# Optimization experiments

Hardware: AMD Instinct MI355X
Metric: run time of the kernel (lower is better)

The kernel has to match this reference:

```python
import jax, jax.numpy as jnp
import numpy as np

NEG_SLOPE = 0.2  # PyG GATConv default leaky_relu slope
EPS = 1e-16     # PyG softmax denominator epsilon


def gat_conv(x, src, dst, edge_attr, W, att_src, att_dst, W_edge, att_edge, bias):
    """Single-head PyG GATConv with edge_dim. x:[N,Fin] -> [N,Fout].
    src/dst already include self-loops; edge_attr matches their length."""
    N = x.shape[0]
    h = x @ W                      # [N, Fout] transformed node features
    a_s = h @ att_src              # [N] per-node source logit contribution
    a_d = h @ att_dst              # [N]
    a_e = (edge_attr @ W_edge) @ att_edge   # [E] edge contribution
    logits = jax.nn.leaky_relu(a_s[src] + a_d[dst] + a_e, NEG_SLOPE)  # [E]
    # segment softmax over destination nodes
    m = jax.ops.segment_max(logits, dst, num_segments=N)    # [N]
    m = jnp.where(jnp.isfinite(m), m, 0.0)
    e = jnp.exp(logits - m[dst])                             # [E]
    denom = jax.ops.segment_sum(e, dst, num_segments=N)      # [N]
    alpha = e / (denom[dst] + EPS)                            # [E]
    # scatter-aggregate weighted messages
    out = jax.ops.segment_sum(alpha[:, None] * h[src], dst, num_segments=N)
    return out + bias


def setup_inputs() -> dict:
    key = jax.random.key(0)
    ks = jax.random.split(key, 16)
    N, E, F_in, H, C, ED = 100000, 1600000, 128, 64, 2, 1
    inp = {
        "x": jax.random.normal(ks[0], (N, F_in), dtype=jnp.float32),
        "edge_index": jax.random.randint(ks[1], (2, E), 0, N, dtype=jnp.int32),
        "edge_attr": jax.random.normal(ks[2], (E, ED), dtype=jnp.float32),
        # layer 1 params (Glorot-ish scale)
        "W1": jax.random.normal(ks[3], (F_in, H), dtype=jnp.float32) * (1.0 / np.sqrt(F_in)),
        "att_src1": jax.random.normal(ks[4], (H,), dtype=jnp.float32) * (1.0 / np.sqrt(H)),
        "att_dst1": jax.random.normal(ks[5], (H,), dtype=jnp.float32) * (1.0 / np.sqrt(H)),
        "W_edge1": jax.random.normal(ks[6], (ED, H), dtype=jnp.float32),
        "att_edge1": jax.random.normal(ks[7], (H,), dtype=jnp.float32) * (1.0 / np.sqrt(H)),
        "bias1": jnp.zeros((H,), dtype=jnp.float32),
        # layer 2 params
        "W2": jax.random.normal(ks[8], (H, C), dtype=jnp.float32) * (1.0 / np.sqrt(H)),
        "att_src2": jax.random.normal(ks[9], (C,), dtype=jnp.float32),
        "att_dst2": jax.random.normal(ks[10], (C,), dtype=jnp.float32),
        "W_edge2": jax.random.normal(ks[11], (ED, C), dtype=jnp.float32),
        "att_edge2": jax.random.normal(ks[12], (C,), dtype=jnp.float32),
        "bias2": jnp.zeros((C,), dtype=jnp.float32),
    }
    return inp


def reference(x, edge_index, edge_attr,
              W1, att_src1, att_dst1, W_edge1, att_edge1, bias1,
              W2, att_src2, att_dst2, W_edge2, att_edge2, bias2):
    N = x.shape[0]
    # PyG GATConv add_self_loops=True, fill_value='mean' for edge_attr
    loop = jnp.arange(N, dtype=edge_index.dtype)
    src = jnp.concatenate([edge_index[0], loop])
    dst = jnp.concatenate([edge_index[1], loop])
    ea_mean = jnp.mean(edge_attr, axis=0, keepdims=True)              # [1, ED]
    ea = jnp.concatenate([edge_attr, jnp.broadcast_to(ea_mean, (N, edge_attr.shape[1]))])

    h = gat_conv(x, src, dst, ea, W1, att_src1, att_dst1, W_edge1, att_edge1, bias1)
    h = jax.nn.relu(h)  # dropout is identity in eval mode
    out = gat_conv(h, src, dst, ea, W2, att_src2, att_dst2, W_edge2, att_edge2, bias2)
    return jax.nn.log_softmax(out, axis=1)
```

## Files before the change

### kernel.cpp

```cpp
#include <hip/hip_runtime.h>
#include <math.h>

#define NEG_SLOPE 0.2f
#define EPSF 1e-16f

constexpr int FIN = 128;
constexpr int H   = 64;
constexpr int C   = 2;
constexpr int BSHIFT = 8;
constexpr int NBUCK_MAX = 1024;
constexpr int CHUNK = 4096;
constexpr int CAP   = 6144;

typedef short v8s __attribute__((ext_vector_type(8)));
typedef float v4f __attribute__((ext_vector_type(4)));
typedef unsigned short u16;

__device__ inline void split_bf16(float v, u16& hi, u16& lo) {
    unsigned u = __float_as_uint(v);
    unsigned r = (u + 0x7FFFu + ((u >> 16) & 1u)) >> 16;
    hi = (u16)r;
    float hf = __uint_as_float(r << 16);
    float l = v - hf;
    unsigned ul = __float_as_uint(l);
    lo = (u16)((ul + 0x7FFFu + ((ul >> 16) & 1u)) >> 16);
}

__device__ inline u16 to_bf16(float v) {
    unsigned u = __float_as_uint(v);
    return (u16)((u + 0x7FFFu + ((u >> 16) & 1u)) >> 16);
}
__device__ inline float blo(int v) { return __uint_as_float((unsigned)v << 16); }
__device__ inline float bhi(int v) { return __uint_as_float((unsigned)v & 0xFFFF0000u); }

__device__ inline int scan1024_excl(int v, int* wtot, int t) {
    int lane = t & 63, w = t >> 6;
    int incl = v;
    #pragma unroll
    for (int o = 1; o < 64; o <<= 1) {
        int u = __shfl_up(incl, o, 64);
        if (lane >= o) incl += u;
    }
    if (lane == 63) wtot[w] = incl;
    __syncthreads();
    int woff = 0;
    for (int i = 0; i < w; i++) woff += wtot[i];
    return woff + incl - v;
}

__global__ __launch_bounds__(1024) void fused_pre_gemm_kernel(
        const float* __restrict__ ea, const int* __restrict__ dst, int E,
        float* __restrict__ csum, int* __restrict__ cnt, int* __restrict__ bcount,
        const float* __restrict__ x, const float* __restrict__ W1,
        const float* __restrict__ att_src, const float* __restrict__ att_dst,
        u16* __restrict__ h1b, float* __restrict__ a_s, float* __restrict__ a_d,
        int N, int NBUCK, int NCHUNK) {
    int t = threadIdx.x;
    if ((int)blockIdx.x < NCHUNK) {
        __shared__ int lh[NBUCK_MAX];
        __shared__ float wsum[16];
        int c = blockIdx.x;
        lh[t] = 0;
        __syncthreads();
        int base = c * CHUNK;
        int cntE = min(CHUNK, E - base);
        float acc = 0.f;
        for (int i = t; i < cntE; i += 1024) {
            int e = base + i;
            acc += ea[e];
            atomicAdd(&lh[dst[e] >> BSHIFT], 1);
        }
        for (int off = 32; off; off >>= 1) acc += __shfl_down(acc, off, 64);
        int lane = t & 63, wv = t >> 6;
        if (lane == 0) wsum[wv] = acc;
        __syncthreads();
        if (t == 0) {
            float s = 0.f;
            #pragma unroll
            for (int i = 0; i < 16; i++) s += wsum[i];
            csum[c] = s;
        }
        if (t < NBUCK) {
            int v = lh[t];
            cnt[(size_t)c * NBUCK + t] = v;
            if (v) atomicAdd(&bcount[t], v);
        }
        return;
    }
    __shared__ u16 WhL[FIN * H];
    __shared__ u16 WlL[FIN * H];
    int bid = blockIdx.x - NCHUNK;
    int w = t >> 6, lane = t & 63;
    int m = lane & 15, q = lane >> 4;
    int base = bid * 256 + w * 16;
    int nodeA = base + m;
    bool inA = nodeA < N;
    const float* xrow = x + (size_t)nodeA * FIN;

    float w1v[8];
    #pragma unroll
    for (int j = 0; j < 8; j++) w1v[j] = W1[t + j * 1024];
    float4 xv4[8];
    #pragma unroll
    for (int kt = 0; kt < 4; kt++) {
        if (inA) {
            const float4* p = (const float4*)(xrow + kt * 32 + q * 8);
            xv4[kt * 2]     = p[0];
            xv4[kt * 2 + 1] = p[1];
        } else {
            xv4[kt * 2]     = make_float4(0.f, 0.f, 0.f, 0.f);
            xv4[kt * 2 + 1] = make_float4(0.f, 0.f, 0.f, 0.f);
        }
    }
    #pragma unroll
    for (int j = 0; j < 8; j++) {
        int gid = t + j * 1024;
        int k = gid >> 6, f = gid & 63;
        u16 hb, lb;
        split_bf16(w1v[j], hb, lb);
        int idx = ((k >> 3) << 9) + (f << 3) + (k & 7);
        WhL[idx] = hb;
        WlL[idx] = lb;
    }
    v8s ah[4], al[4];
    #pragma unroll
    for (int kt = 0; kt < 4; kt++) {
        float xv[8];
        xv[0] = xv4[kt * 2].x;     xv[1] = xv4[kt * 2].y;
        xv[2] = xv4[kt * 2].z;     xv[3] = xv4[kt * 2].w;
        xv[4] = xv4[kt * 2 + 1].x; xv[5] = xv4[kt * 2 + 1].y;
        xv[6] = xv4[kt * 2 + 1].z; xv[7] = xv4[kt * 2 + 1].w;
        #pragma unroll
        for (int j = 0; j < 8; j++) {
            u16 hb, lb;
            split_bf16(xv[j], hb, lb);
            ah[kt][j] = (short)hb;
            al[kt][j] = (short)lb;
        }
    }
    __syncthreads();

    float ps[4] = {0.f, 0.f, 0.f, 0.f};
    float pd[4] = {0.f, 0.f, 0.f, 0.f};
    #pragma unroll
    for (int ft = 0; ft < 4; ft++) {
        v4f acc = {0.f, 0.f, 0.f, 0.f};
        #pragma unroll
        for (int kt = 0; kt < 4; kt++) {
            int fi = ((kt * 4 + q) << 9) + ((ft * 16 + m) << 3);
            v8s bh = *(const v8s*)(WhL + fi);
            v8s bl = *(const v8s*)(WlL + fi);
            acc = __builtin_amdgcn_mfma_f32_16x16x32_bf16(ah[kt], bh, acc, 0, 0, 0);
            acc = __builtin_amdgcn_mfma_f32_16x16x32_bf16(al[kt], bh, acc, 0, 0, 0);
            acc = __builtin_amdgcn_mfma_f32_16x16x32_bf16(ah[kt], bl, acc, 0, 0, 0);
        }
        int f = ft * 16 + m;
        float asf = att_src[f], adf = att_dst[f];
        #pragma unroll
        for (int r = 0; r < 4; r++) {
            int node = base + q * 4 + r;
            if (node < N) h1b[(size_t)node * H + f] = to_bf16(acc[r]);
            ps[r] += acc[r] * asf;
            pd[r] += acc[r] * adf;
        }
    }
    #pragma unroll
    for (int msk = 1; msk < 16; msk <<= 1) {
        #pragma unroll
        for (int r = 0; r < 4; r++) {
            ps[r] += __shfl_xor(ps[r], msk, 64);
            pd[r] += __shfl_xor(pd[r], msk, 64);
        }
    }
    if (m == 0) {
        #pragma unroll
        for (int r = 0; r < 4; r++) {
            int node = base + q * 4 + r;
            if (node < N) { a_s[node] = ps[r]; a_d[node] = pd[r]; }
        }
    }
}

__global__ __launch_bounds__(1024) void stage_kernel(
        const int* __restrict__ src, const int* __restrict__ dst, const float* __restrict__ ea,
        int E, const int* __restrict__ cnt, const int* __restrict__ bcount,
        int* __restrict__ gcur,
        int2* __restrict__ staging, int* __restrict__ bbase_out, int NBUCK, int NCHUNK,
        const float* __restrict__ csum,
        const float* __restrict__ W_edge1, const float* __restrict__ att_edge1,
        const float* __restrict__ W_edge2, const float* __restrict__ att_edge2,
        float* __restrict__ scal, int* __restrict__ rowN) {
    __shared__ int   bb[NBUCK_MAX];
    __shared__ int   cur[NBUCK_MAX];
    __shared__ int   gofs[NBUCK_MAX];
    __shared__ int2  sbuf[CHUNK];
    __shared__ short sbkt[CHUNK];
    __shared__ int   wt16[16];
    __shared__ float ws16[16];
    int t = threadIdx.x;
    int c = blockIdx.x;
    int base = c * CHUNK;
    int cntE = min(CHUNK, E - base);
    int bv = (t < NBUCK) ? bcount[t] : 0;
    int bx = scan1024_excl(bv, wt16, t);
    if (t < NBUCK) bb[t] = bx;
    if (c == 0) {
        if (t < NBUCK) bbase_out[t] = bx;
        if (t == 0) { bbase_out[NBUCK] = E; *rowN = E; }
        float acc = 0.f;
        for (int i = t; i < NCHUNK; i += 1024) acc += csum[i];
        for (int off = 32; off; off >>= 1) acc += __shfl_down(acc, off, 64);
        if ((t & 63) == 0) ws16[t >> 6] = acc;
    }
    __syncthreads();
    if (c == 0 && t == 0) {
        float tot = 0.f;
        #pragma unroll
        for (int i = 0; i < 16; i++) tot += ws16[i];
        float c1 = 0.f;
        for (int i = 0; i < H; i++) c1 += W_edge1[i] * att_edge1[i];
        float c2 = 0.f;
        for (int i = 0; i < C; i++) c2 += W_edge2[i] * att_edge2[i];
        scal[0] = tot / (float)E; scal[1] = c1; scal[2] = c2;
    }
    int h = (t < NBUCK) ? cnt[(size_t)c * NBUCK + t] : 0;
    int p = scan1024_excl(h, wt16, t);
    if (t < NBUCK) {
        if (h) gofs[t] = bb[t] + atomicAdd(&gcur[t], h) - p;
        cur[t] = p;
    }
    __syncthreads();
    for (int i = t; i < cntE; i += 1024) {
        int e = base + i;
        int d = dst[e];
        int b = d >> BSHIFT;
        int slot = atomicAdd(&cur[b], 1);
        sbuf[slot] = make_int2(src[e] | ((d & ((1 << BSHIFT) - 1)) << 20), __float_as_int(ea[e]));
        sbkt[slot] = (short)b;
    }
    __syncthreads();
    for (int j = t; j < cntE; j += 1024)
        staging[gofs[sbkt[j]] + j] = sbuf[j];
}

__global__ __launch_bounds__(1024) void bfin_kernel(
        const int2* __restrict__ staging, const int* __restrict__ bbase,
        const float* __restrict__ scal,
        const float* __restrict__ a_s1, const float* __restrict__ a_d1,
        int* __restrict__ row, int2* __restrict__ sedge, float* __restrict__ sea2, int N) {
    __shared__ int   nh[256];
    __shared__ int   wt16[16];
    __shared__ int2  ebuf[CAP];
    __shared__ float abuf[CAP];
    int b = blockIdx.x, t = threadIdx.x;
    int beg = bbase[b], end = bbase[b + 1];
    int cnt = end - beg;
    int node0 = b << BSHIFT;
    float c1 = scal[1];
    if (t < 256) nh[t] = 0;
    __syncthreads();
    for (int i = beg + t; i < end; i += 1024)
        atomicAdd(&nh[(unsigned)staging[i].x >> 20], 1);
    __syncthreads();
    int v = (t < 256) ? nh[t] : 0;
    int lane = t & 63, w = t >> 6;
    int incl = v;
    #pragma unroll
    for (int o = 1; o < 64; o <<= 1) {
        int u = __shfl_up(incl, o, 64);
        if (lane >= o) incl += u;
    }
    if (w < 4 && lane == 63) wt16[w] = incl;
    __syncthreads();
    int woff = 0;
    int wl = w < 4 ? w : 4;
    for (int i = 0; i < wl; i++) woff += wt16[i];
    int excl = woff + incl - v;
    int node = node0 + t;
    if (t < 256 && node < N) row[node] = beg + excl;
    bool fast = (cnt <= CAP);
    if (t < 256) nh[t] = fast ? excl : beg + excl;
    __syncthreads();
    for (int i = beg + t; i < end; i += 1024) {
        int2 r = staging[i];
        int dlow = (unsigned)r.x >> 20;
        int sn = r.x & 0xFFFFF;
        float eav = __int_as_float(r.y);
        float lg = a_s1[sn] + a_d1[node0 + dlow] + eav * c1;
        lg = lg > 0.f ? lg : NEG_SLOPE * lg;
        float ex = __expf(lg);
        int pos = atomicAdd(&nh[dlow], 1);
        if (fast) {
            ebuf[pos] = make_int2(sn, __float_as_int(ex));
            abuf[pos] = eav;
        } else {
            sedge[pos] = make_int2(sn, __float_as_int(ex));
            sea2[pos] = eav;
        }
    }
    __syncthreads();
    if (fast) {
        for (int j = t; j < cnt; j += 1024) {
            sedge[beg + j] = ebuf[j];
            sea2[beg + j]  = abuf[j];
        }
    }
}

__device__ inline void accum8(float acc[8], float& den, float xw, int4 hv) {
    den += xw;
    acc[0] += xw * blo(hv.x); acc[1] += xw * bhi(hv.x);
    acc[2] += xw * blo(hv.y); acc[3] += xw * bhi(hv.y);
    acc[4] += xw * blo(hv.z); acc[5] += xw * bhi(hv.z);
    acc[6] += xw * blo(hv.w); acc[7] += xw * bhi(hv.w);
}

__global__ __launch_bounds__(256) void agg1_kernel(
        const int* __restrict__ row, const int2* __restrict__ sedge,
        const float* __restrict__ scal,
        const float* __restrict__ a_s, const float* __restrict__ a_d,
        const u16* __restrict__ h1b,
        const float* __restrict__ bias1, const float* __restrict__ W2,
        const float* __restrict__ att_src2, const float* __restrict__ att_dst2,
        float* __restrict__ h2, float* __restrict__ a_s2, float* __restrict__ a_d2,
        int N) {
    int wv = threadIdx.x >> 6;
    int lane = threadIdx.x & 63;
    int g  = lane >> 3;
    int fl = lane & 7;
    int n = blockIdx.x * 32 + wv * 8 + g;
    if (n >= N) return;
    int beg = row[n], end = row[n + 1];
    float den = 0.f;
    float acc[8] = {0.f, 0.f, 0.f, 0.f, 0.f, 0.f, 0.f, 0.f};
    const u16* hrow = h1b + fl * 8;
    int i = beg;
    for (; i + 4 <= end; i += 4) {
        int2 e0 = sedge[i], e1 = sedge[i + 1], e2 = sedge[i + 2], e3 = sedge[i + 3];
        int4 h0 = *(const int4*)(hrow + (size_t)e0.x * H);
        int4 h1v = *(const int4*)(hrow + (size_t)e1.x * H);
        int4 h2v = *(const int4*)(hrow + (size_t)e2.x * H);
        int4 h3v = *(const int4*)(hrow + (size_t)e3.x * H);
        accum8(acc, den, __int_as_float(e0.y), h0);
        accum8(acc, den, __int_as_float(e1.y), h1v);
        accum8(acc, den, __int_as_float(e2.y), h2v);
        accum8(acc, den, __int_as_float(e3.y), h3v);
    }
    if (i + 2 <= end) {
        int2 e0 = sedge[i], e1 = sedge[i + 1];
        int4 h0 = *(const int4*)(hrow + (size_t)e0.x * H);
        int4 h1v = *(const int4*)(hrow + (size_t)e1.x * H);
        accum8(acc, den, __int_as_float(e0.y), h0);
        accum8(acc, den, __int_as_float(e1.y), h1v);
        i += 2;
    }
    if (i < end) {
        int2 e0 = sedge[i];
        int4 h0 = *(const int4*)(hrow + (size_t)e0.x * H);
        accum8(acc, den, __int_as_float(e0.y), h0);
    }
    {
        float lg = a_s[n] + a_d[n] + scal[0] * scal[1];
        lg = lg > 0.f ? lg : NEG_SLOPE * lg;
        float ex = __expf(lg);
        int4 hs = *(const int4*)(hrow + (size_t)n * H);
        accum8(acc, den, ex, hs);
    }
    float inv = 1.f / (den + EPSF);
    float p0 = 0.f, p1 = 0.f;
    #pragma unroll
    for (int k = 0; k < 8; k++) {
        int f = fl * 8 + k;
        float hr = acc[k] * inv + bias1[f];
        hr = fmaxf(hr, 0.f);
        p0 += hr * W2[f * C + 0];
        p1 += hr * W2[f * C + 1];
    }
    #pragma unroll
    for (int msk = 1; msk < 8; msk <<= 1) {
        p0 += __shfl_xor(p0, msk, 64);
        p1 += __shfl_xor(p1, msk, 64);
    }
    if (fl == 0) {
        h2[(size_t)n * C + 0] = p0;
        h2[(size_t)n * C + 1] = p1;
        a_s2[n] = p0 * att_src2[0] + p1 * att_src2[1];
        a_d2[n] = p0 * att_dst2[0] + p1 * att_dst2[1];
    }
}

__global__ __launch_bounds__(256) void agg2_kernel(
        const int* __restrict__ row, const int2* __restrict__ sedge, const float* __restrict__ sea2,
        const float* __restrict__ scal,
        const float* __restrict__ a_s2, const float* __restrict__ a_d2,
        const float* __restrict__ h2, const float* __restrict__ bias2,
        float* __restrict__ out, int N) {
    int wv = threadIdx.x >> 6;
    int lane = threadIdx.x & 63;
    int g  = lane >> 3;
    int fl = lane & 7;
    int n = blockIdx.x * 32 + wv * 8 + g;
    if (n >= N) return;
    float c2 = scal[2];
    float ad = a_d2[n];
    int beg = row[n], end = row[n + 1];
    float den = 0.f, m0 = 0.f, m1 = 0.f;
    for (int i = beg + fl; i < end; i += 8) {
        int s = sedge[i].x;
        float lg = a_s2[s] + ad + sea2[i] * c2;
        lg = lg > 0.f ? lg : NEG_SLOPE * lg;
        float ex = __expf(lg);
        den += ex;
        m0 += ex * h2[(size_t)s * C + 0];
        m1 += ex * h2[(size_t)s * C + 1];
    }
    if (fl == 0) {
        float lg = a_s2[n] + ad + scal[0] * c2;
        lg = lg > 0.f ? lg : NEG_SLOPE * lg;
        float ex = __expf(lg);
        den += ex;
        m0 += ex * h2[(size_t)n * C + 0];
        m1 += ex * h2[(size_t)n * C + 1];
    }
    #pragma unroll
    for (int msk = 1; msk < 8; msk <<= 1) {
        den += __shfl_xor(den, msk, 64);
        m0  += __shfl_xor(m0, msk, 64);
        m1  += __shfl_xor(m1, msk, 64);
    }
    if (fl == 0) {
        float dn = den + EPSF;
        float o0 = m0 / dn + bias2[0];
        float o1 = m1 / dn + bias2[1];
        float mx = fmaxf(o0, o1);
        float lse = mx + logf(expf(o0 - mx) + expf(o1 - mx));
        out[(size_t)n * C + 0] = o0 - lse;
        out[(size_t)n * C + 1] = o1 - lse;
    }
}

extern "C" void kernel_launch(void* const* d_in, const int* in_sizes, int n_in,
                              void* d_out, int out_size, void* d_ws, size_t ws_size,
                              hipStream_t stream) {
    const float* x        = (const float*)d_in[0];
    const int*   ei       = (const int*)d_in[1];
    const float* ea       = (const float*)d_in[2];
    const float* W1       = (const float*)d_in[3];
    const float* att_src1 = (const float*)d_in[4];
    const float* att_dst1 = (const float*)d_in[5];
    const float* W_edge1  = (const float*)d_in[6];
    const float* att_edge1= (const float*)d_in[7];
    const float* bias1    = (const float*)d_in[8];
    const float* W2       = (const float*)d_in[9];
    const float* att_src2 = (const float*)d_in[10];
    const float* att_dst2 = (const float*)d_in[11];
    const float* W_edge2  = (const float*)d_in[12];
    const float* att_edge2= (const float*)d_in[13];
    const float* bias2    = (const float*)d_in[14];

    const int N  = in_sizes[0] / FIN;
    const int E  = in_sizes[1] / 2;
    const int* srcp = ei;
    const int* dstp = ei + E;
    const int NBUCK  = (N + (1 << BSHIFT) - 1) >> BSHIFT;
    const int NCHUNK = (E + CHUNK - 1) / CHUNK;
    const int NGEMM  = (N + 255) / 256;

    char* wsb = (char*)d_ws;
    size_t off = 0;
    auto alloc = [&](size_t bytes) { void* p = wsb + off; off += (bytes + 255) & ~size_t(255); return p; };
    int*   bcount = (int*)alloc((size_t)NBUCK_MAX * 4);
    int*   gcur   = (int*)alloc((size_t)NBUCK_MAX * 4);
    size_t zbytes = off;
    float* csum   = (float*)alloc((size_t)2048 * 4);
    int*   bbase  = (int*)alloc((size_t)(NBUCK_MAX + 1) * 4);
    int*   cnt    = (int*)alloc((size_t)NCHUNK * NBUCK * 4);
    int*   row    = (int*)alloc((size_t)(N + 1) * 4);
    int2*  sedge  = (int2*)alloc((size_t)(E + 8) * 8);
    float* sea2   = (float*)alloc((size_t)E * 4);
    int2*  staging= (int2*)alloc((size_t)E * 8);
    u16*   h1b    = (u16*)alloc((size_t)N * H * 2);
    float* a_s1   = (float*)alloc((size_t)N * 4);
    float* a_d1   = (float*)alloc((size_t)N * 4);
    float* h2     = (float*)alloc((size_t)N * C * 4);
    float* a_s2   = (float*)alloc((size_t)N * 4);
    float* a_d2   = (float*)alloc((size_t)N * 4);
    float* scal   = (float*)alloc(3 * 4);

    hipMemsetAsync(d_ws, 0, zbytes, stream);

    fused_pre_gemm_kernel<<<NCHUNK + NGEMM, 1024, 0, stream>>>(
        ea, dstp, E, csum, cnt, bcount,
        x, W1, att_src1, att_dst1, h1b, a_s1, a_d1, N, NBUCK, NCHUNK);
    stage_kernel<<<NCHUNK, 1024, 0, stream>>>(
        srcp, dstp, ea, E, cnt, bcount, gcur, staging, bbase, NBUCK, NCHUNK,
        csum, W_edge1, att_edge1, W_edge2, att_edge2, scal, row + N);
    bfin_kernel<<<NBUCK, 1024, 0, stream>>>(staging, bbase, scal, a_s1, a_d1, row, sedge, sea2, N);
    agg1_kernel<<<(N + 31) / 32, 256, 0, stream>>>(row, sedge, scal, a_s1, a_d1, h1b,
                                                   bias1, W2, att_src2, att_dst2,
                                                   h2, a_s2, a_d2, N);
    agg2_kernel<<<(N + 31) / 32, 256, 0, stream>>>(row, sedge, sea2, scal, a_s2, a_d2, h2, bias2,
                                                   (float*)d_out, N);
}
```

Before: 226.8 us.

## Split layer-1 GEMM into separate 256-thread kernel with pre-split bf16 weights

The layer-1 MFMA GEMM no longer shares a launch with the histogram blocks. The pre kernel now writes W1 once to global memory as hi/lo bf16 halves in MFMA layout, and a new 256-thread GEMM kernel copies those halves into LDS with vector loads. This removes the per-block W1 split and lets smaller blocks raise occupancy. In exchange it adds a kernel launch, puts the GEMM after the staging kernel instead of overlapping it with the histogram, and each block still loads 32KB of weights for only 64 nodes.

```diff
diff --git a/kernel.cpp b/kernel.cpp
--- a/kernel.cpp
+++ b/kernel.cpp
@@ -48,136 +48,49 @@
     return woff + incl - v;
 }
 
-__global__ __launch_bounds__(1024) void fused_pre_gemm_kernel(
-        const float* __restrict__ ea, const int* __restrict__ dst, int E,
-        float* __restrict__ csum, int* __restrict__ cnt, int* __restrict__ bcount,
-        const float* __restrict__ x, const float* __restrict__ W1,
-        const float* __restrict__ att_src, const float* __restrict__ att_dst,
-        u16* __restrict__ h1b, float* __restrict__ a_s, float* __restrict__ a_d,
-        int N, int NBUCK, int NCHUNK) {
-    int t = threadIdx.x;
-    if ((int)blockIdx.x < NCHUNK) {
-        __shared__ int lh[NBUCK_MAX];
-        __shared__ float wsum[16];
-        int c = blockIdx.x;
-        lh[t] = 0;
-        __syncthreads();
-        int base = c * CHUNK;
-        int cntE = min(CHUNK, E - base);
-        float acc = 0.f;
-        for (int i = t; i < cntE; i += 1024) {
-            int e = base + i;
-            acc += ea[e];
-            atomicAdd(&lh[dst[e] >> BSHIFT], 1);
-        }
-        for (int off = 32; off; off >>= 1) acc += __shfl_down(acc, off, 64);
-        int lane = t & 63, wv = t >> 6;
-        if (lane == 0) wsum[wv] = acc;
-        __syncthreads();
-        if (t == 0) {
-            float s = 0.f;
-            #pragma unroll
-            for (int i = 0; i < 16; i++) s += wsum[i];
-            csum[c] = s;
-        }
-        if (t < NBUCK) {
-            int v = lh[t];
-            cnt[(size_t)c * NBUCK + t] = v;
-            if (v) atomicAdd(&bcount[t], v);
-        }
-        return;
-    }
-    __shared__ u16 WhL[FIN * H];
-    __shared__ u16 WlL[FIN * H];
-    int bid = blockIdx.x - NCHUNK;
-    int w = t >> 6, lane = t & 63;
-    int m = lane & 15, q = lane >> 4;
-    int base = bid * 256 + w * 16;
-    int nodeA = base + m;
-    bool inA = nodeA < N;
-    const float* xrow = x + (size_t)nodeA * FIN;
-
-    float w1v[8];
-    #pragma unroll
-    for (int j = 0; j < 8; j++) w1v[j] = W1[t + j * 1024];
-    float4 xv4[8];
-    #pragma unroll
-    for (int kt = 0; kt < 4; kt++) {
-        if (inA) {
-            const float4* p = (const float4*)(xrow + kt * 32 + q * 8);
-            xv4[kt * 2]     = p[0];
-            xv4[kt * 2 + 1] = p[1];
-        } else {
-            xv4[kt * 2]     = make_float4(0.f, 0.f, 0.f, 0.f);
-            xv4[kt * 2 + 1] = make_float4(0.f, 0.f, 0.f, 0.f);
-        }
-    }
-    #pragma unroll
-    for (int j = 0; j < 8; j++) {
-        int gid = t + j * 1024;
+__global__ __launch_bounds__(1024) void pre_kernel(const float* __restrict__ ea,
+                                                   const int* __restrict__ dst, int E,
+                                                   float* __restrict__ csum, int* __restrict__ cnt,
+                                                   int* __restrict__ bcount,
+                                                   const float* __restrict__ W1,
+                                                   u16* __restrict__ Wt_hi, u16* __restrict__ Wt_lo,
+                                                   int NBUCK) {
+    int c = blockIdx.x, t = threadIdx.x;
+    int gid = c * 1024 + t;
+    if (gid < FIN * H) {
         int k = gid >> 6, f = gid & 63;
-        u16 hb, lb;
-        split_bf16(w1v[j], hb, lb);
+        u16 h, l;
+        split_bf16(W1[gid], h, l);
         int idx = ((k >> 3) << 9) + (f << 3) + (k & 7);
-        WhL[idx] = hb;
-        WlL[idx] = lb;
-    }
-    v8s ah[4], al[4];
-    #pragma unroll
-    for (int kt = 0; kt < 4; kt++) {
-        float xv[8];
-        xv[0] = xv4[kt * 2].x;     xv[1] = xv4[kt * 2].y;
-        xv[2] = xv4[kt * 2].z;     xv[3] = xv4[kt * 2].w;
-        xv[4] = xv4[kt * 2 + 1].x; xv[5] = xv4[kt * 2 + 1].y;
-        xv[6] = xv4[kt * 2 + 1].z; xv[7] = xv4[kt * 2 + 1].w;
-        #pragma unroll
-        for (int j = 0; j < 8; j++) {
-            u16 hb, lb;
-            split_bf16(xv[j], hb, lb);
-            ah[kt][j] = (short)hb;
-            al[kt][j] = (short)lb;
-        }
-    }
-    __syncthreads();
-
-    float ps[4] = {0.f, 0.f, 0.f, 0.f};
-    float pd[4] = {0.f, 0.f, 0.f, 0.f};
-    #pragma unroll
-    for (int ft = 0; ft < 4; ft++) {
-        v4f acc = {0.f, 0.f, 0.f, 0.f};
-        #pragma unroll
-        for (int kt = 0; kt < 4; kt++) {
-            int fi = ((kt * 4 + q) << 9) + ((ft * 16 + m) << 3);
-            v8s bh = *(const v8s*)(WhL + fi);
-            v8s bl = *(const v8s*)(WlL + fi);
-            acc = __builtin_amdgcn_mfma_f32_16x16x32_bf16(ah[kt], bh, acc, 0, 0, 0);
-            acc = __builtin_amdgcn_mfma_f32_16x16x32_bf16(al[kt], bh, acc, 0, 0, 0);
-            acc = __builtin_amdgcn_mfma_f32_16x16x32_bf16(ah[kt], bl, acc, 0, 0, 0);
-        }
-        int f = ft * 16 + m;
-        float asf = att_src[f], adf = att_dst[f];
-        #pragma unroll
-        for (int r = 0; r < 4; r++) {
-            int node = base + q * 4 + r;
-            if (node < N) h1b[(size_t)node * H + f] = to_bf16(acc[r]);
-            ps[r] += acc[r] * asf;
-            pd[r] += acc[r] * adf;
-        }
-    }
-    #pragma unroll
-    for (int msk = 1; msk < 16; msk <<= 1) {
-        #pragma unroll
-        for (int r = 0; r < 4; r++) {
-            ps[r] += __shfl_xor(ps[r], msk, 64);
-            pd[r] += __shfl_xor(pd[r], msk, 64);
-        }
-    }
-    if (m == 0) {
-        #pragma unroll
-        for (int r = 0; r < 4; r++) {
-            int node = base + q * 4 + r;
-            if (node < N) { a_s[node] = ps[r]; a_d[node] = pd[r]; }
-        }
+        Wt_hi[idx] = h;
+        Wt_lo[idx] = l;
+    }
+    __shared__ int lh[NBUCK_MAX];
+    __shared__ float wsum[16];
+    lh[t] = 0;
+    __syncthreads();
+    int base = c * CHUNK;
+    int cntE = min(CHUNK, E - base);
+    float acc = 0.f;
+    for (int i = t; i < cntE; i += 1024) {
+        int e = base + i;
+        acc += ea[e];
+        atomicAdd(&lh[dst[e] >> BSHIFT], 1);
+    }
+    for (int off = 32; off; off >>= 1) acc += __shfl_down(acc, off, 64);
+    int lane = t & 63, wv = t >> 6;
+    if (lane == 0) wsum[wv] = acc;
+    __syncthreads();
+    if (t == 0) {
+        float s = 0.f;
+        #pragma unroll
+        for (int i = 0; i < 16; i++) s += wsum[i];
+        csum[c] = s;
+    }
+    if (t < NBUCK) {
+        int v = lh[t];
+        cnt[(size_t)c * NBUCK + t] = v;
+        if (v) atomicAdd(&bcount[t], v);
     }
 }
 
@@ -243,6 +156,112 @@
         staging[gofs[sbkt[j]] + j] = sbuf[j];
 }
 
+__global__ __launch_bounds__(256) void gemm1_mfma_kernel(
+        const float* __restrict__ x,
+        const u16* __restrict__ Wt_hi, const u16* __restrict__ Wt_lo,
+        const float* __restrict__ att_src, const float* __restrict__ att_dst,
+        u16* __restrict__ h1b, float* __restrict__ a_s, float* __restrict__ a_d, int N) {
+    __shared__ u16 WhL[FIN * H];
+    __shared__ u16 WlL[FIN * H];
+    int t = threadIdx.x;
+    int w = t >> 6, lane = t & 63;
+    int m = lane & 15, q = lane >> 4;
+    int base = blockIdx.x * 64 + w * 16;
+    int nodeA = base + m;
+    bool inA = nodeA < N;
+    const float* xrow = x + (size_t)nodeA * FIN;
+
+    float4 fh[4], fl4[4];
+    {
+        const float4* gh = (const float4*)Wt_hi;
+        const float4* gl = (const float4*)Wt_lo;
+        #pragma unroll
+        for (int i = 0; i < 4; i++) {
+            fh[i]  = gh[t + i * 256];
+            fl4[i] = gl[t + i * 256];
+        }
+    }
+    float4 xv4[8];
+    #pragma unroll
+    for (int kt = 0; kt < 4; kt++) {
+        if (inA) {
+            const float4* p = (const float4*)(xrow + kt * 32 + q * 8);
+            xv4[kt * 2]     = p[0];
+            xv4[kt * 2 + 1] = p[1];
+        } else {
+            xv4[kt * 2]     = make_float4(0.f, 0.f, 0.f, 0.f);
+            xv4[kt * 2 + 1] = make_float4(0.f, 0.f, 0.f, 0.f);
+        }
+    }
+    {
+        float4* sh = (float4*)WhL;
+        float4* sl = (float4*)WlL;
+        #pragma unroll
+        for (int i = 0; i < 4; i++) {
+            sh[t + i * 256] = fh[i];
+            sl[t + i * 256] = fl4[i];
+        }
+    }
+
+    v8s ah[4], al[4];
+    #pragma unroll
+    for (int kt = 0; kt < 4; kt++) {
+        float xv[8];
+        xv[0] = xv4[kt * 2].x;     xv[1] = xv4[kt * 2].y;
+        xv[2] = xv4[kt * 2].z;     xv[3] = xv4[kt * 2].w;
+        xv[4] = xv4[kt * 2 + 1].x; xv[5] = xv4[kt * 2 + 1].y;
+        xv[6] = xv4[kt * 2 + 1].z; xv[7] = xv4[kt * 2 + 1].w;
+        #pragma unroll
+        for (int j = 0; j < 8; j++) {
+            u16 hb, lb;
+            split_bf16(xv[j], hb, lb);
+            ah[kt][j] = (short)hb;
+            al[kt][j] = (short)lb;
+        }
+    }
+    __syncthreads();
+
+    float ps[4] = {0.f, 0.f, 0.f, 0.f};
+    float pd[4] = {0.f, 0.f, 0.f, 0.f};
+    #pragma unroll
+    for (int ft = 0; ft < 4; ft++) {
+        v4f acc = {0.f, 0.f, 0.f, 0.f};
+        #pragma unroll
+        for (int kt = 0; kt < 4; kt++) {
+            int fi = ((kt * 4 + q) << 9) + ((ft * 16 + m) << 3);
+            v8s bh = *(const v8s*)(WhL + fi);
+            v8s bl = *(const v8s*)(WlL + fi);
+            acc = __builtin_amdgcn_mfma_f32_16x16x32_bf16(ah[kt], bh, acc, 0, 0, 0);
+            acc = __builtin_amdgcn_mfma_f32_16x16x32_bf16(al[kt], bh, acc, 0, 0, 0);
+            acc = __builtin_amdgcn_mfma_f32_16x16x32_bf16(ah[kt], bl, acc, 0, 0, 0);
+        }
+        int f = ft * 16 + m;
+        float asf = att_src[f], adf = att_dst[f];
+        #pragma unroll
+        for (int r = 0; r < 4; r++) {
+            int node = base + q * 4 + r;
+            if (node < N) h1b[(size_t)node * H + f] = to_bf16(acc[r]);
+            ps[r] += acc[r] * asf;
+            pd[r] += acc[r] * adf;
+        }
+    }
+    #pragma unroll
+    for (int msk = 1; msk < 16; msk <<= 1) {
+        #pragma unroll
+        for (int r = 0; r < 4; r++) {
+            ps[r] += __shfl_xor(ps[r], msk, 64);
+            pd[r] += __shfl_xor(pd[r], msk, 64);
+        }
+    }
+    if (m == 0) {
+        #pragma unroll
+        for (int r = 0; r < 4; r++) {
+            int node = base + q * 4 + r;
+            if (node < N) { a_s[node] = ps[r]; a_d[node] = pd[r]; }
+        }
+    }
+}
+
 __global__ __launch_bounds__(1024) void bfin_kernel(
         const int2* __restrict__ staging, const int* __restrict__ bbase,
         const float* __restrict__ scal,
@@ -464,7 +483,6 @@
     const int* dstp = ei + E;
     const int NBUCK  = (N + (1 << BSHIFT) - 1) >> BSHIFT;
     const int NCHUNK = (E + CHUNK - 1) / CHUNK;
-    const int NGEMM  = (N + 255) / 256;
 
     char* wsb = (char*)d_ws;
     size_t off = 0;
@@ -480,6 +498,8 @@
     float* sea2   = (float*)alloc((size_t)E * 4);
     int2*  staging= (int2*)alloc((size_t)E * 8);
     u16*   h1b    = (u16*)alloc((size_t)N * H * 2);
+    u16*   Wt_hi  = (u16*)alloc((size_t)FIN * H * 2);
+    u16*   Wt_lo  = (u16*)alloc((size_t)FIN * H * 2);
     float* a_s1   = (float*)alloc((size_t)N * 4);
     float* a_d1   = (float*)alloc((size_t)N * 4);
     float* h2     = (float*)alloc((size_t)N * C * 4);
@@ -489,12 +509,13 @@
 
     hipMemsetAsync(d_ws, 0, zbytes, stream);
 
-    fused_pre_gemm_kernel<<<NCHUNK + NGEMM, 1024, 0, stream>>>(
-        ea, dstp, E, csum, cnt, bcount,
-        x, W1, att_src1, att_dst1, h1b, a_s1, a_d1, N, NBUCK, NCHUNK);
+    pre_kernel<<<NCHUNK, 1024, 0, stream>>>(ea, dstp, E, csum, cnt, bcount,
+                                            W1, Wt_hi, Wt_lo, NBUCK);
     stage_kernel<<<NCHUNK, 1024, 0, stream>>>(
         srcp, dstp, ea, E, cnt, bcount, gcur, staging, bbase, NBUCK, NCHUNK,
         csum, W_edge1, att_edge1, W_edge2, att_edge2, scal, row + N);
+    gemm1_mfma_kernel<<<(N + 63) / 64, 256, 0, stream>>>(x, Wt_hi, Wt_lo, att_src1, att_dst1,
+                                                         h1b, a_s1, a_d1, N);
     bfin_kernel<<<NBUCK, 1024, 0, stream>>>(staging, bbase, scal, a_s1, a_d1, row, sedge, sea2, N);
     agg1_kernel<<<(N + 31) / 32, 256, 0, stream>>>(row, sedge, scal, a_s1, a_d1, h1b,
                                                    bias1, W2, att_src2, att_dst2,
```

After: 222.5 us. Within noise of the previous version (-1.9%).
